# Kernel optimization log

Hardware: AMD Instinct MI355X
Metric: run time of the kernel (lower is better)

The kernel has to match this reference:

```python
import jax, jax.numpy as jnp
import numpy as np

C = 384          # input_channels
DH = 768         # dim_hidden
WS = 7           # window size (kernel_size)
NH = 12          # num_heads
HID = 3072       # mlp hidden = dim_hidden * mlp_ratio
NP = WS * WS     # 49 patch tokens
N = NP + 1       # + 1 cls token
SCALE = (C // NH) ** -0.5
REL_DIM = 2 * WS - 1


def _rel_pos_index():
    r = np.arange(WS)
    qx, qy = np.meshgrid(r, r, indexing='ij')
    q = np.stack([qx.ravel(), qy.ravel()], -1)                 # [NP,2], row-major flatten
    rel = q[:, None, :] - q[None, :, :] + WS - 1               # [NP,NP,2], values in [0,2ws-2]
    return jnp.asarray(rel[..., 0] * REL_DIM + rel[..., 1])    # [NP,NP]

REL_IDX = _rel_pos_index()


def layer_norm(x, g, b, eps=1e-5):
    m = jnp.mean(x, axis=-1, keepdims=True)
    v = jnp.var(x, axis=-1, keepdims=True)
    return (x - m) * jax.lax.rsqrt(v + eps) * g + b


def attention(x, w_qkv, w_proj, b_proj, rel_pos=None, mask=None):
    Bx, Nx, Cx = x.shape
    qkv = (x @ w_qkv.T).reshape(Bx, Nx, 3, NH, Cx // NH).transpose(2, 0, 3, 1, 4)
    q, k, v = qkv[0], qkv[1], qkv[2]                           # [B,H,N,d]
    attn = jnp.einsum('bhqd,bhkd->bhqk', q, k) * SCALE
    if rel_pos is not None:
        bias = rel_pos[REL_IDX].transpose(2, 0, 1)[None]       # [1,NH,NP,NP]
        attn = attn.at[:, :, 1:, 1:].add(bias)                 # skip cls token row/col
    if mask is not None:
        attn = attn + mask[:, None]                            # broadcast over heads
    attn = jax.nn.softmax(attn, axis=-1)
    y = jnp.einsum('bhqk,bhkd->bhqd', attn, v).transpose(0, 2, 1, 3).reshape(Bx, Nx, Cx)
    return y @ w_proj.T + b_proj


def setup_inputs() -> dict:
    key = jax.random.key(0)
    ks = jax.random.split(key, 16)
    s = 0.02
    BNW = 2048  # B * num_windows = 32 * 64
    return {
        'out': jax.random.normal(ks[0], (BNW, N, C), jnp.float32),
        'mask': jnp.zeros((BNW, N, N), jnp.float32),
        'g0': jnp.ones((C,), jnp.float32), 'b0': jnp.zeros((C,), jnp.float32),
        'g1': jnp.ones((C,), jnp.float32), 'b1': jnp.zeros((C,), jnp.float32),
        'g2': jnp.ones((C,), jnp.float32), 'b2': jnp.zeros((C,), jnp.float32),
        'ge': jnp.ones((C,), jnp.float32), 'be': jnp.zeros((C,), jnp.float32),
        'w_qkv': jax.random.normal(ks[1], (3 * C, C), jnp.float32) * s,
        'w_proj': jax.random.normal(ks[2], (C, C), jnp.float32) * s,
        'b_proj': jnp.zeros((C,), jnp.float32),
        'rel_pos': jax.random.normal(ks[3], (REL_DIM * REL_DIM, NH), jnp.float32) * s,
        'w_fc1': jax.random.normal(ks[4], (HID, C), jnp.float32) * s,
        'b_fc1': jnp.zeros((HID,), jnp.float32),
        'w_fc2': jax.random.normal(ks[5], (DH, HID), jnp.float32) * s,
        'b_fc2': jnp.zeros((DH,), jnp.float32),
        'w_exp': jax.random.normal(ks[6], (DH, C), jnp.float32) * s,
        'b_exp': jnp.zeros((DH,), jnp.float32),
        'w_lin': jax.random.normal(ks[7], (C, DH), jnp.float32) * s,
        'b_lin': jnp.zeros((C,), jnp.float32),
        'B': 32, 'H': 56, 'W': 56,
    }


def reference(out, mask, g0, b0, g1, b1, g2, b2, ge, be,
              w_qkv, w_proj, b_proj, rel_pos,
              w_fc1, b_fc1, w_fc2, b_fc2, w_exp, b_exp, w_lin, b_lin,
              B, H, W):
    Cc = out.shape[-1]
    # cls-token attention across windows of each image
    cls = out[:, :1].reshape(B, -1, Cc)                        # [B, nw, C]
    cls = cls + attention(layer_norm(cls, g0, b0), w_qkv, w_proj, b_proj)
    cls = cls.reshape(-1, 1, Cc)
    x = jnp.concatenate([cls, out[:, 1:]], axis=1)             # [B*nw, N, C]
    # windowed patch attention with rel-pos bias + mask
    x = x + attention(layer_norm(x, g1, b1), w_qkv, w_proj, b_proj,
                      rel_pos=rel_pos, mask=mask)
    # expand path: norm -> gelu -> linear (input_channels != dim_hidden)
    identity = jax.nn.gelu(layer_norm(x, ge, be), approximate=False) @ w_exp.T + b_exp
    # mlp path: norm -> fc1 -> gelu -> fc2
    h = layer_norm(x, g2, b2)
    h = jax.nn.gelu(h @ w_fc1.T + b_fc1, approximate=False)
    h = h @ w_fc2.T + b_fc2
    tmp = identity + h                                          # [B*nw, N, DH]
    return tmp @ w_lin.T + b_lin                                # [B*nw, N, C]
```

## Files before the change

### kernel.cpp

```cpp
#include <hip/hip_runtime.h>
#include <hip/hip_bf16.h>
#include <math.h>

#define NHEADS 12
#define NTOK   50
#define NWIN   2048
#define IMGS   32
#define CDIM   384
#define QKVD   1152
#define DHID   768
#define MLPH   3072
#define KTAIL  3456
#define SCALE_F 0.17677669529663687f

typedef short short8 __attribute__((ext_vector_type(8)));
typedef short short4v __attribute__((ext_vector_type(4)));
typedef short short2v __attribute__((ext_vector_type(2)));
typedef float f32x4  __attribute__((ext_vector_type(4)));
typedef __hip_bfloat16 bf16;

__device__ __forceinline__ float gelu_f(float x){
  return 0.5f*x*(1.0f+erff(x*0.7071067811865476f));
}
__device__ __forceinline__ short bfs(float x){
  bf16 h = __float2bfloat16(x); return *(short*)&h;
}

__global__ void cvt4_kernel(const float* s0, bf16* d0, int n0,
                            const float* s1, bf16* d1, int n1,
                            const float* s2, bf16* d2, int n2,
                            const float* s3, bf16* d3, int n3){
  int stride = gridDim.x*blockDim.x, g = blockIdx.x*blockDim.x + threadIdx.x;
  for (int i=g; i<n0; i+=stride) d0[i] = __float2bfloat16(s0[i]);
  for (int i=g; i<n1; i+=stride) d1[i] = __float2bfloat16(s1[i]);
  for (int i=g; i<n2; i+=stride) d2[i] = __float2bfloat16(s2[i]);
  for (int i=g; i<n3; i+=stride) d3[i] = __float2bfloat16(s3[i]);
}

__global__ __launch_bounds__(256) void transpose_cvt_kernel(const float* __restrict__ src,
    bf16* __restrict__ dst, int R, int Cc){
  __shared__ float tile[32][33];
  int bx = blockIdx.x, by = blockIdx.y;
  int c = threadIdx.x & 31, r0 = threadIdx.x >> 5;
  #pragma unroll
  for (int rr = r0; rr < 32; rr += 8)
    tile[rr][c] = src[(size_t)(by*32+rr)*Cc + bx*32 + c];
  __syncthreads();
  #pragma unroll
  for (int rr = r0; rr < 32; rr += 8)
    dst[(size_t)(bx*32+rr)*R + by*32 + c] = __float2bfloat16(tile[c][rr]);
}

__global__ void bias_combine_kernel(const float* __restrict__ wlin,
    const float* __restrict__ b_lin, const float* __restrict__ b_exp,
    const float* __restrict__ b_fc2, float* __restrict__ biasc){
  int i = blockIdx.x*blockDim.x + threadIdx.x;
  if (i >= CDIM) return;
  float s = b_lin[i];
  for (int d=0; d<DHID; d++) s += wlin[(size_t)i*DHID+d]*(b_exp[d]+b_fc2[d]);
  biasc[i] = s;
}

template<bool GELU>
__global__ __launch_bounds__(256) void ln_kernel(const float* __restrict__ x, long ldx,
    const float* __restrict__ g, const float* __restrict__ b,
    bf16* __restrict__ y, int rows)
{
  int row = blockIdx.x*4 + (threadIdx.x>>6);
  if (row >= rows) return;
  int l = threadIdx.x & 63;
  const float2* xr = (const float2*)(x + (size_t)row*ldx);
  float2 v[3]; float s = 0.f;
  #pragma unroll
  for (int j=0;j<3;j++){ v[j] = xr[l + 64*j]; s += v[j].x + v[j].y; }
  #pragma unroll
  for (int off=32; off; off>>=1) s += __shfl_xor(s, off, 64);
  float mean = s * (1.0f/384.0f);
  float vs = 0.f;
  #pragma unroll
  for (int j=0;j<3;j++){ float dx=v[j].x-mean, dy=v[j].y-mean; vs += dx*dx+dy*dy; }
  #pragma unroll
  for (int off=32; off; off>>=1) vs += __shfl_xor(vs, off, 64);
  float rstd = rsqrtf(vs*(1.0f/384.0f) + 1e-5f);
  short2v* yr = (short2v*)(y + (size_t)row*384);
  const float2* gv = (const float2*)g; const float2* bv = (const float2*)b;
  #pragma unroll
  for (int j=0;j<3;j++){
    float2 gg = gv[l+64*j], bb = bv[l+64*j];
    float o0 = (v[j].x-mean)*rstd*gg.x + bb.x;
    float o1 = (v[j].y-mean)*rstd*gg.y + bb.y;
    if (GELU){ o0 = gelu_f(o0); o1 = gelu_f(o1); }
    short2v pk; pk[0]=bfs(o0); pk[1]=bfs(o1);
    yr[l+64*j] = pk;
  }
}

__global__ __launch_bounds__(256) void ln_dual_kernel(const float* __restrict__ x,
    const float* __restrict__ ge, const float* __restrict__ be,
    const float* __restrict__ g2, const float* __restrict__ b2,
    bf16* __restrict__ yeo, long lde, bf16* __restrict__ y2o, int rows)
{
  int row = blockIdx.x*4 + (threadIdx.x>>6);
  if (row >= rows) return;
  int l = threadIdx.x & 63;
  const float2* xr = (const float2*)(x + (size_t)row*384);
  float2 v[3]; float s = 0.f;
  #pragma unroll
  for (int j=0;j<3;j++){ v[j] = xr[l + 64*j]; s += v[j].x + v[j].y; }
  #pragma unroll
  for (int off=32; off; off>>=1) s += __shfl_xor(s, off, 64);
  float mean = s * (1.0f/384.0f);
  float vs = 0.f;
  #pragma unroll
  for (int j=0;j<3;j++){ float dx=v[j].x-mean, dy=v[j].y-mean; vs += dx*dx+dy*dy; }
  #pragma unroll
  for (int off=32; off; off>>=1) vs += __shfl_xor(vs, off, 64);
  float rstd = rsqrtf(vs*(1.0f/384.0f) + 1e-5f);
  short2v* ye = (short2v*)(yeo + (size_t)row*lde);
  short2v* y2 = (short2v*)(y2o + (size_t)row*384);
  const float2* gev = (const float2*)ge; const float2* bev = (const float2*)be;
  const float2* g2v = (const float2*)g2; const float2* b2v = (const float2*)b2;
  #pragma unroll
  for (int j=0;j<3;j++){
    float n0 = (v[j].x-mean)*rstd, n1 = (v[j].y-mean)*rstd;
    float2 gg = gev[l+64*j], bb = bev[l+64*j];
    short2v pe; pe[0]=bfs(gelu_f(n0*gg.x+bb.x)); pe[1]=bfs(gelu_f(n1*gg.y+bb.y));
    ye[l+64*j] = pe;
    gg = g2v[l+64*j]; bb = b2v[l+64*j];
    short2v p2; p2[0]=bfs(n0*gg.x+bb.x); p2[1]=bfs(n1*gg.y+bb.y);
    y2[l+64*j] = p2;
  }
}

template<bool OUT_BF16, bool BIAS, int RES, bool GELU>
__device__ __forceinline__ void gemm_dev(
    const bf16* __restrict__ A, const bf16* __restrict__ B, void* Cv,
    const float* __restrict__ bias, const void* res,
    int M, int N, int K, int ldc, int ldres)
{
  __shared__ short As[3][128*32];
  __shared__ short Bs[3][128*32];
  const int t  = threadIdx.x;
  const int l  = t & 63;
  const int w  = t >> 6;
  const int wr = w >> 1, wc = w & 1;
  const int lr = l & 15, kg = l >> 4;

  const int nwg = gridDim.x * gridDim.y;
  const int lin = blockIdx.y * gridDim.x + blockIdx.x;
  const int q8 = nwg >> 3, r8 = nwg & 7;
  const int xcd = lin & 7, slot = lin >> 3;
  const int swz = (xcd < r8) ? (xcd*(q8+1) + slot) : (r8*(q8+1) + (xcd-r8)*q8 + slot);
  const int by = swz / gridDim.x, bx = swz - by*gridDim.x;

  const int bm = by * 128, bn = bx * 128;
  const short* Ag = (const short*)A;
  const short* Bg = (const short*)B;

  const int eo0 = w*1024 + l*8;
  const int rowS0 = eo0 >> 5, colS0 = eo0 & 31;
  const int eo1 = eo0 + 512;
  const int rowS1 = eo1 >> 5, colS1 = eo1 & 31;

  #define STAGE(k0, b) do { \
    __builtin_amdgcn_global_load_lds( \
      (const __attribute__((address_space(1))) void*)&Ag[(size_t)(bm+rowS0)*K + (k0) + colS0], \
      (__attribute__((address_space(3))) void*)((char*)&As[b][0] + w*2048), 16, 0, 0); \
    __builtin_amdgcn_global_load_lds( \
      (const __attribute__((address_space(1))) void*)&Bg[(size_t)(bn+rowS0)*K + (k0) + colS0], \
      (__attribute__((address_space(3))) void*)((char*)&Bs[b][0] + w*2048), 16, 0, 0); \
    __builtin_amdgcn_global_load_lds( \
      (const __attribute__((address_space(1))) void*)&Ag[(size_t)(bm+rowS1)*K + (k0) + colS1], \
      (__attribute__((address_space(3))) void*)((char*)&As[b][0] + w*2048 + 1024), 16, 0, 0); \
    __builtin_amdgcn_global_load_lds( \
      (const __attribute__((address_space(1))) void*)&Bg[(size_t)(bn+rowS1)*K + (k0) + colS1], \
      (__attribute__((address_space(3))) void*)((char*)&Bs[b][0] + w*2048 + 1024), 16, 0, 0); \
  } while(0)

  f32x4 acc[4][4] = {};

  STAGE(0, 0);
  STAGE(32, 1);
  asm volatile("s_waitcnt vmcnt(4)" ::: "memory");
  __builtin_amdgcn_s_barrier();

  int cur = 0, nb = 2;
  for (int k0 = 0; k0 < K; k0 += 32) {
    const bool more = (k0 + 64 < K);
    if (more) STAGE(k0 + 64, nb);

    short8 af[4], bfm[4];
    #pragma unroll
    for (int m=0;m<4;m++) af[m]  = *(const short8*)(&As[cur][(wr*64 + m*16 + lr)*32 + kg*8]);
    #pragma unroll
    for (int n=0;n<4;n++) bfm[n] = *(const short8*)(&Bs[cur][(wc*64 + n*16 + lr)*32 + kg*8]);
    __builtin_amdgcn_s_setprio(1);
    #pragma unroll
    for (int m=0;m<4;m++)
      #pragma unroll
      for (int n=0;n<4;n++)
        acc[m][n] = __builtin_amdgcn_mfma_f32_16x16x32_bf16(af[m], bfm[n], acc[m][n], 0,0,0);
    __builtin_amdgcn_s_setprio(0);

    if (more) { asm volatile("s_waitcnt vmcnt(4)" ::: "memory"); }
    else      { asm volatile("s_waitcnt vmcnt(0)" ::: "memory"); }
    __builtin_amdgcn_s_barrier();
    cur = (cur==2) ? 0 : cur+1;
    nb  = (nb==2)  ? 0 : nb+1;
  }
  #undef STAGE

  #pragma unroll
  for (int m=0;m<4;m++){
    int row0 = bm + wr*64 + m*16 + kg*4;
    #pragma unroll
    for (int n=0;n<4;n++){
      int col = bn + wc*64 + n*16 + lr;
      float bv = BIAS ? bias[col] : 0.0f;
      #pragma unroll
      for (int r=0;r<4;r++){
        float val = acc[m][n][r] + bv;
        if (RES == 1) val += ((const float*)res)[(size_t)(row0+r)*ldres + col];
        if (GELU) val = gelu_f(val);
        if (OUT_BF16) ((bf16*)Cv)[(size_t)(row0+r)*ldc + col] = __float2bfloat16(val);
        else          ((float*)Cv)[(size_t)(row0+r)*ldc + col] = val;
      }
    }
  }
}

#define GEMM_K(NAME, OB, BI, RE, GE) \
__global__ __launch_bounds__(256) void NAME( \
    const bf16* __restrict__ A, const bf16* __restrict__ B, void* Cv, \
    const float* __restrict__ bias, const void* res, \
    int M, int N, int K, int ldc, int ldres){ \
  gemm_dev<OB,BI,RE,GE>(A,B,Cv,bias,res,M,N,K,ldc,ldres); }

GEMM_K(gemm_qkv_k,  true,  false, 0, false)
GEMM_K(gemm_proj_k, false, true,  1, false)
GEMM_K(gemm_fc1_k,  true,  true,  0, true)
GEMM_K(gemm_tail_k, false, true,  0, false)
GEMM_K(gemm_wcmb_k, true,  false, 0, false)

__global__ __launch_bounds__(256) void attn_cls_kernel(const bf16* __restrict__ qkv,
                                                       bf16* __restrict__ y)
{
  int img = blockIdx.x, h = blockIdx.y;
  __shared__ float q[64][33], k[64][33], v[64][33];
  __shared__ float s[64][65];
  int t = threadIdx.x;
  for (int idx=t; idx<64*32; idx+=256){
    int i = idx>>5, d = idx&31;
    const bf16* base = qkv + ((size_t)(img*64+i))*QKVD + h*32 + d;
    q[i][d] = __bfloat162float(base[0]);
    k[i][d] = __bfloat162float(base[384]);
    v[i][d] = __bfloat162float(base[768]);
  }
  __syncthreads();
  for (int idx=t; idx<64*64; idx+=256){
    int i = idx>>6, j = idx&63;
    float a = 0.f;
    #pragma unroll
    for (int d=0; d<32; d++) a += q[i][d]*k[j][d];
    s[i][j] = a * SCALE_F;
  }
  __syncthreads();
  if (t < 64){
    float m = -1e30f;
    for (int j=0;j<64;j++) m = fmaxf(m, s[t][j]);
    float sum = 0.f;
    for (int j=0;j<64;j++){ float e = __expf(s[t][j]-m); s[t][j]=e; sum+=e; }
    float inv = 1.0f/sum;
    for (int j=0;j<64;j++) s[t][j] *= inv;
  }
  __syncthreads();
  for (int idx=t; idx<64*32; idx+=256){
    int i = idx>>5, d = idx&31;
    float a = 0.f;
    for (int j=0;j<64;j++) a += s[i][j]*v[j][d];
    y[((size_t)(img*64+i))*CDIM + h*32 + d] = __float2bfloat16(a);
  }
}

__global__ __launch_bounds__(64) void attn_win_mfma(const bf16* __restrict__ qkv,
    const float* __restrict__ mask, const float* __restrict__ rel_pos,
    bf16* __restrict__ y)
{
  const int lw = blockIdx.x, h = blockIdx.y;
  const int l = threadIdx.x;
  const int lr = l & 15, kg = l >> 4;
  __shared__ short Plds[64*72];
  __shared__ short VTl[32*72];
  __shared__ float rp[169];

  const size_t tok0 = (size_t)lw * NTOK;
  const short* qbase = (const short*)qkv;

  for (int i=l; i<169; i+=64) rp[i] = rel_pos[i*NHEADS + h];

  short8 qf[4], kf[4];
  #pragma unroll
  for (int n=0;n<4;n++){
    int qt = 16*n + lr;
    if (qt < 50) qf[n] = *(const short8*)&qbase[(tok0+qt)*QKVD + h*32 + kg*8];
    else         qf[n] = short8(0);
  }
  #pragma unroll
  for (int m=0;m<4;m++){
    int kt = 16*m + lr;
    if (kt < 50) kf[m] = *(const short8*)&qbase[(tok0+kt)*QKVD + 384 + h*32 + kg*8];
    else         kf[m] = short8(0);
  }

  {
    short vv[32];
    if (l < 50){
      const short8* vp = (const short8*)&qbase[(tok0+l)*QKVD + 768 + h*32];
      #pragma unroll
      for (int jj=0;jj<4;jj++){ short8 xv = vp[jj];
        #pragma unroll
        for (int e=0;e<8;e++) vv[jj*8+e] = xv[e]; }
    } else {
      #pragma unroll
      for (int d=0; d<32; d++) vv[d]=0;
    }
    #pragma unroll
    for (int d=0; d<32; d++) VTl[d*72 + l] = vv[d];
  }

  f32x4 sacc[4][4] = {};
  #pragma unroll
  for (int m=0;m<4;m++)
    #pragma unroll
    for (int n=0;n<4;n++)
      sacc[m][n] = __builtin_amdgcn_mfma_f32_16x16x32_bf16(kf[m], qf[n], sacc[m][n], 0,0,0);

  const float* mrow = mask + (size_t)lw*2500;
  float sv[4][4][4];
  #pragma unroll
  for (int m=0;m<4;m++){
    #pragma unroll
    for (int r=0;r<4;r++){
      int kt = 16*m + 4*kg + r;
      #pragma unroll
      for (int n=0;n<4;n++){
        int qt = 16*n + lr;
        float a;
        if (kt < 50 && qt < 50){
          a = sacc[m][n][r] * SCALE_F;
          if (kt>=1 && qt>=1){
            int qi=qt-1, kj=kt-1;
            int ridx = ((qi/7)-(kj/7)+6)*13 + (qi%7)-(kj%7)+6;
            a += rp[ridx];
          }
          a += mrow[qt*50+kt];
        } else a = -1e30f;
        sv[m][r][n] = a;
      }
    }
  }

  #pragma unroll
  for (int n=0;n<4;n++){
    float mx = -1e30f;
    #pragma unroll
    for (int m=0;m<4;m++)
      #pragma unroll
      for (int r=0;r<4;r++) mx = fmaxf(mx, sv[m][r][n]);
    mx = fmaxf(mx, __shfl_xor(mx, 16));
    mx = fmaxf(mx, __shfl_xor(mx, 32));
    float sum = 0.f;
    float pv[4][4];
    #pragma unroll
    for (int m=0;m<4;m++)
      #pragma unroll
      for (int r=0;r<4;r++){ float p = __expf(sv[m][r][n]-mx); pv[m][r]=p; sum+=p; }
    sum += __shfl_xor(sum, 16);
    sum += __shfl_xor(sum, 32);
    float inv = 1.0f/sum;
    int qrow = (16*n + lr)*72;
    #pragma unroll
    for (int m=0;m<4;m++){
      short4v pk;
      #pragma unroll
      for (int r=0;r<4;r++) pk[r] = bfs(pv[m][r]*inv);
      *(short4v*)&Plds[qrow + 16*m + 4*kg] = pk;
    }
  }
  __syncthreads();

  f32x4 oacc[2][4] = {};
  #pragma unroll
  for (int ks=0; ks<2; ks++){
    short8 pf[4];
    #pragma unroll
    for (int n=0;n<4;n++)
      pf[n] = *(const short8*)&Plds[(16*n+lr)*72 + 32*ks + kg*8];
    #pragma unroll
    for (int md=0; md<2; md++){
      short8 vf = *(const short8*)&VTl[(16*md+lr)*72 + 32*ks + kg*8];
      #pragma unroll
      for (int n=0;n<4;n++)
        oacc[md][n] = __builtin_amdgcn_mfma_f32_16x16x32_bf16(vf, pf[n], oacc[md][n], 0,0,0);
    }
  }

  short* yb = (short*)y;
  #pragma unroll
  for (int n=0;n<4;n++){
    int qt = 16*n + lr;
    if (qt >= 50) continue;
    #pragma unroll
    for (int md=0; md<2; md++){
      short4v pk;
      #pragma unroll
      for (int r=0;r<4;r++) pk[r] = bfs(oacc[md][n][r]);
      *(short4v*)&yb[(tok0+qt)*CDIM + h*32 + 16*md + 4*kg] = pk;
    }
  }
}

extern "C" void kernel_launch(void* const* d_in, const int* in_sizes, int n_in,
                              void* d_out, int out_size, void* d_ws, size_t ws_size,
                              hipStream_t stream)
{
  const float* x_in   = (const float*)d_in[0];
  const float* maskp  = (const float*)d_in[1];
  const float* g0 = (const float*)d_in[2];  const float* b0 = (const float*)d_in[3];
  const float* g1 = (const float*)d_in[4];  const float* b1 = (const float*)d_in[5];
  const float* g2 = (const float*)d_in[6];  const float* b2 = (const float*)d_in[7];
  const float* ge = (const float*)d_in[8];  const float* be = (const float*)d_in[9];
  const float* w_qkv = (const float*)d_in[10];
  const float* w_proj= (const float*)d_in[11];
  const float* b_proj= (const float*)d_in[12];
  const float* rel_pos=(const float*)d_in[13];
  const float* w_fc1 = (const float*)d_in[14];
  const float* b_fc1 = (const float*)d_in[15];
  const float* w_fc2 = (const float*)d_in[16];
  const float* b_fc2 = (const float*)d_in[17];
  const float* w_exp = (const float*)d_in[18];
  const float* b_exp = (const float*)d_in[19];
  const float* w_lin = (const float*)d_in[20];
  const float* b_lin = (const float*)d_in[21];
  float* dout = (float*)d_out;

  const size_t NT = (size_t)NWIN * NTOK;

  size_t off = 0;
  auto alloc = [&](size_t bytes)->void* {
    void* p = (char*)d_ws + off;
    off += (bytes + 255) & ~(size_t)255;
    return p;
  };

  bf16* wqkv_b = (bf16*)alloc((size_t)QKVD*CDIM*2);
  bf16* wproj_b= (bf16*)alloc((size_t)CDIM*CDIM*2);
  bf16* wfc1_b = (bf16*)alloc((size_t)MLPH*CDIM*2);
  bf16* wlin_b = (bf16*)alloc((size_t)CDIM*DHID*2);
  bf16* wexpT_b= (bf16*)alloc((size_t)CDIM*DHID*2);
  bf16* wfc2T_b= (bf16*)alloc((size_t)MLPH*DHID*2);
  bf16* W_comb = (bf16*)alloc((size_t)CDIM*KTAIL*2);
  float* biasc = (float*)alloc((size_t)CDIM*4);
  float* xb    = (float*)alloc(NT*CDIM*4);
  bf16* clsln  = (bf16*)alloc((size_t)NWIN*CDIM*2);
  bf16* qkvcls = (bf16*)alloc((size_t)NWIN*QKVD*2);
  bf16* ycls   = (bf16*)alloc((size_t)NWIN*CDIM*2);

  int CH_W = 2048;
  const size_t per_window = 537600ull;
  while (CH_W > 128 && off + (size_t)CH_W*per_window + 16384 > ws_size) CH_W >>= 1;
  const int CH_T = CH_W * NTOK;

  bf16*  xln   = (bf16*) alloc((size_t)CH_T*CDIM*2);
  bf16*  qkvc  = (bf16*) alloc((size_t)CH_T*QKVD*2);
  bf16*  ybfc  = (bf16*) alloc((size_t)CH_T*CDIM*2);
  bf16*  h1ext = (bf16*) alloc((size_t)CH_T*KTAIL*2);

  cvt4_kernel<<<512, 256, 0, stream>>>(
      w_qkv, wqkv_b, QKVD*CDIM,  w_proj, wproj_b, CDIM*CDIM,
      w_fc1, wfc1_b, MLPH*CDIM,  w_lin,  wlin_b,  CDIM*DHID);
  transpose_cvt_kernel<<<dim3(CDIM/32, DHID/32), 256, 0, stream>>>(w_exp, wexpT_b, DHID, CDIM);
  transpose_cvt_kernel<<<dim3(MLPH/32, DHID/32), 256, 0, stream>>>(w_fc2, wfc2T_b, DHID, MLPH);
  bias_combine_kernel<<<6, 64, 0, stream>>>(w_lin, b_lin, b_exp, b_fc2, biasc);
  gemm_wcmb_k<<<dim3(CDIM/128, CDIM/128), 256, 0, stream>>>(
      wlin_b, wexpT_b, W_comb, nullptr, nullptr, CDIM, CDIM, DHID, KTAIL, 0);
  gemm_wcmb_k<<<dim3(MLPH/128, CDIM/128), 256, 0, stream>>>(
      wlin_b, wfc2T_b, W_comb + 384, nullptr, nullptr, CDIM, MLPH, DHID, KTAIL, 0);

  hipMemcpyAsync(xb, x_in, NT*CDIM*4, hipMemcpyDeviceToDevice, stream);

  ln_kernel<false><<<NWIN/4, 256, 0, stream>>>(x_in, (long)NTOK*CDIM, g0, b0, clsln, NWIN);
  gemm_qkv_k<<<dim3(QKVD/128, NWIN/128), 256, 0, stream>>>(
      clsln, wqkv_b, qkvcls, nullptr, nullptr, NWIN, QKVD, CDIM, QKVD, 0);
  attn_cls_kernel<<<dim3(IMGS, NHEADS), 256, 0, stream>>>(qkvcls, ycls);
  gemm_proj_k<<<dim3(CDIM/128, NWIN/128), 256, 0, stream>>>(
      ycls, wproj_b, xb, b_proj, x_in, NWIN, CDIM, CDIM, NTOK*CDIM, NTOK*CDIM);

  const int nch = NWIN / CH_W;
  for (int c = 0; c < nch; c++){
    int w0 = c * CH_W;
    size_t t0 = (size_t)w0 * NTOK;
    float* xbc = xb + t0*CDIM;
    float* doutc = dout + t0*CDIM;
    int MT = CH_T, MB = CH_T/128;

    ln_kernel<false><<<MT/4, 256, 0, stream>>>(xbc, CDIM, g1, b1, xln, MT);
    gemm_qkv_k<<<dim3(QKVD/128, MB), 256, 0, stream>>>(
        xln, wqkv_b, qkvc, nullptr, nullptr, MT, QKVD, CDIM, QKVD, 0);
    attn_win_mfma<<<dim3(CH_W, NHEADS), 64, 0, stream>>>(
        qkvc, maskp + (size_t)w0*2500, rel_pos, ybfc);
    gemm_proj_k<<<dim3(CDIM/128, MB), 256, 0, stream>>>(
        ybfc, wproj_b, xbc, b_proj, xbc, MT, CDIM, CDIM, CDIM, CDIM);

    ln_dual_kernel<<<MT/4, 256, 0, stream>>>(xbc, ge, be, g2, b2, h1ext, KTAIL, ybfc, MT);

    gemm_fc1_k<<<dim3(MLPH/128, MB), 256, 0, stream>>>(
        ybfc, wfc1_b, h1ext + 384, b_fc1, nullptr, MT, MLPH, CDIM, KTAIL, 0);

    gemm_tail_k<<<dim3(CDIM/128, MB), 256, 0, stream>>>(
        h1ext, W_comb, doutc, biasc, nullptr, MT, CDIM, KTAIL, CDIM, 0);
  }
}
```

Measured before the change: 1.826 ms.

## Deepen GEMM LDS pipeline to five stages and use tanh-approximated GELU

Makes the bf16 MFMA GEMM prefetch four K-tiles ahead through a five-buffer LDS ring instead of two ahead in three buffers, with an explicit drain at the end. The aim is to hide more global-load latency. It also raises LDS use to 80 KB per block, which can cut occupancy. Separately, the exact erf GELU is replaced by the tanh approximation computed with __expf, which is cheaper but numerically differs from the reference's exact GELU.

```diff
diff --git a/kernel.cpp b/kernel.cpp
--- a/kernel.cpp
+++ b/kernel.cpp
@@ -20,7 +20,9 @@
 typedef __hip_bfloat16 bf16;
 
 __device__ __forceinline__ float gelu_f(float x){
-  return 0.5f*x*(1.0f+erff(x*0.7071067811865476f));
+  float z = 0.7978845608028654f*(x + 0.044715f*x*x*x);
+  float e = __expf(2.0f*z);
+  return 0.5f*x*(1.0f + (1.0f - 2.0f/(e+1.0f)));
 }
 __device__ __forceinline__ short bfs(float x){
   bf16 h = __float2bfloat16(x); return *(short*)&h;
@@ -138,8 +140,8 @@
     const float* __restrict__ bias, const void* res,
     int M, int N, int K, int ldc, int ldres)
 {
-  __shared__ short As[3][128*32];
-  __shared__ short Bs[3][128*32];
+  __shared__ short As[5][128*32];
+  __shared__ short Bs[5][128*32];
   const int t  = threadIdx.x;
   const int l  = t & 63;
   const int w  = t >> 6;
@@ -177,38 +179,52 @@
       (__attribute__((address_space(3))) void*)((char*)&Bs[b][0] + w*2048 + 1024), 16, 0, 0); \
   } while(0)
 
+  #define COMPUTE(buf) do { \
+    short8 af[4], bfm[4]; \
+    _Pragma("unroll") \
+    for (int m=0;m<4;m++) af[m]  = *(const short8*)(&As[buf][(wr*64 + m*16 + lr)*32 + kg*8]); \
+    _Pragma("unroll") \
+    for (int n=0;n<4;n++) bfm[n] = *(const short8*)(&Bs[buf][(wc*64 + n*16 + lr)*32 + kg*8]); \
+    __builtin_amdgcn_s_setprio(1); \
+    _Pragma("unroll") \
+    for (int m=0;m<4;m++) \
+      _Pragma("unroll") \
+      for (int n=0;n<4;n++) \
+        acc[m][n] = __builtin_amdgcn_mfma_f32_16x16x32_bf16(af[m], bfm[n], acc[m][n], 0,0,0); \
+    __builtin_amdgcn_s_setprio(0); \
+  } while(0)
+
   f32x4 acc[4][4] = {};
-
-  STAGE(0, 0);
-  STAGE(32, 1);
+  const int nt = K >> 5;
+
+  STAGE(0, 0); STAGE(32, 1); STAGE(64, 2); STAGE(96, 3);
+  asm volatile("s_waitcnt vmcnt(12)" ::: "memory");
+  __builtin_amdgcn_s_barrier();
+
+  int cur = 0;
+  for (int tt = 0; tt < nt-4; ++tt){
+    int nb = cur+4; if (nb >= 5) nb -= 5;
+    STAGE((tt+4)*32, nb);
+    COMPUTE(cur);
+    asm volatile("s_waitcnt vmcnt(12)" ::: "memory");
+    __builtin_amdgcn_s_barrier();
+    cur = (cur==4) ? 0 : cur+1;
+  }
+  COMPUTE(cur);
+  asm volatile("s_waitcnt vmcnt(8)" ::: "memory");
+  __builtin_amdgcn_s_barrier();
+  cur = (cur==4) ? 0 : cur+1;
+  COMPUTE(cur);
   asm volatile("s_waitcnt vmcnt(4)" ::: "memory");
   __builtin_amdgcn_s_barrier();
-
-  int cur = 0, nb = 2;
-  for (int k0 = 0; k0 < K; k0 += 32) {
-    const bool more = (k0 + 64 < K);
-    if (more) STAGE(k0 + 64, nb);
-
-    short8 af[4], bfm[4];
-    #pragma unroll
-    for (int m=0;m<4;m++) af[m]  = *(const short8*)(&As[cur][(wr*64 + m*16 + lr)*32 + kg*8]);
-    #pragma unroll
-    for (int n=0;n<4;n++) bfm[n] = *(const short8*)(&Bs[cur][(wc*64 + n*16 + lr)*32 + kg*8]);
-    __builtin_amdgcn_s_setprio(1);
-    #pragma unroll
-    for (int m=0;m<4;m++)
-      #pragma unroll
-      for (int n=0;n<4;n++)
-        acc[m][n] = __builtin_amdgcn_mfma_f32_16x16x32_bf16(af[m], bfm[n], acc[m][n], 0,0,0);
-    __builtin_amdgcn_s_setprio(0);
-
-    if (more) { asm volatile("s_waitcnt vmcnt(4)" ::: "memory"); }
-    else      { asm volatile("s_waitcnt vmcnt(0)" ::: "memory"); }
-    __builtin_amdgcn_s_barrier();
-    cur = (cur==2) ? 0 : cur+1;
-    nb  = (nb==2)  ? 0 : nb+1;
-  }
+  cur = (cur==4) ? 0 : cur+1;
+  COMPUTE(cur);
+  asm volatile("s_waitcnt vmcnt(0)" ::: "memory");
+  __builtin_amdgcn_s_barrier();
+  cur = (cur==4) ? 0 : cur+1;
+  COMPUTE(cur);
   #undef STAGE
+  #undef COMPUTE
 
   #pragma unroll
   for (int m=0;m<4;m++){
```

After: 2.140 ms. 1.17x slower.

## Add 256-row 512-thread GEMM kernels and switch GELU to tanh approximation

Applied to the files above, without the earlier changes.

Adds a new GEMM template with 256-row tiles, 8 waves, triple-buffered direct global-to-LDS loads, and a 256-wide N tile for fc1. It replaces the 128x128 GEMMs in the per-chunk loop (qkv, proj, fc1, tail) to raise data reuse per block and reduce block count. Separately, GELU is changed from exact erf to the tanh approximation via exp, which cuts epilogue cost but departs from the reference's approximate=False semantics. Larger tiles halve the number of M blocks, which may hurt occupancy or tail balance if chunk sizes are small.

```diff
diff --git a/kernel.cpp b/kernel.cpp
--- a/kernel.cpp
+++ b/kernel.cpp
@@ -20,7 +20,9 @@
 typedef __hip_bfloat16 bf16;
 
 __device__ __forceinline__ float gelu_f(float x){
-  return 0.5f*x*(1.0f+erff(x*0.7071067811865476f));
+  float z = 0.7978845608028654f*(x + 0.044715f*x*x*x);
+  float e = __expf(2.0f*z);
+  return 0.5f*x*(1.0f + (1.0f - 2.0f/(e+1.0f)));
 }
 __device__ __forceinline__ short bfs(float x){
   bf16 h = __float2bfloat16(x); return *(short*)&h;
@@ -131,6 +133,135 @@
     y2[l+64*j] = p2;
   }
 }
+
+template<int BN, bool OUT_BF16, bool BIAS, int RES, bool GELU>
+__device__ __forceinline__ void g256_dev(
+    const bf16* __restrict__ A, const bf16* __restrict__ B, void* Cv,
+    const float* __restrict__ bias, const void* res,
+    int M, int N, int K, int ldc, int ldres)
+{
+  constexpr int WN    = BN/64;
+  constexpr int WM    = 8/WN;
+  constexpr int MREP  = 256/(16*WM);
+  constexpr int BINST = BN/128;
+  constexpr int V     = 2 + BINST;
+
+  __shared__ short As[3][256*32];
+  __shared__ short Bs[3][BN*32];
+
+  const int t  = threadIdx.x;
+  const int l  = t & 63;
+  const int w  = t >> 6;
+  const int wr = w / WN, wc = w % WN;
+  const int lr = l & 15, kg = l >> 4;
+  const int wrow = wr * (MREP*16);
+
+  const int nwg = gridDim.x * gridDim.y;
+  const int lin = blockIdx.y * gridDim.x + blockIdx.x;
+  const int q8 = nwg >> 3, r8 = nwg & 7;
+  const int xcd = lin & 7, slot = lin >> 3;
+  const int swz = (xcd < r8) ? (xcd*(q8+1) + slot) : (r8*(q8+1) + (xcd-r8)*q8 + slot);
+  const int by = swz / gridDim.x, bx = swz - by*gridDim.x;
+  const int bm = by * 256, bn = bx * BN;
+
+  const short* Ag = (const short*)A;
+  const short* Bg = (const short*)B;
+
+  const int srow = l >> 2;
+  const int scol = ((l&3) ^ ((l>>3)&3)) * 8;
+
+  #define STAGE(k0, b) do { \
+    _Pragma("unroll") \
+    for (int p=0;p<2;p++){ \
+      int j = w*2+p; \
+      __builtin_amdgcn_global_load_lds( \
+        (const __attribute__((address_space(1))) void*)&Ag[(size_t)(bm + j*16 + srow)*K + (k0) + scol], \
+        (__attribute__((address_space(3))) void*)((char*)&As[b][0] + j*1024), 16, 0, 0); \
+    } \
+    _Pragma("unroll") \
+    for (int p=0;p<BINST;p++){ \
+      int j = w*BINST+p; \
+      __builtin_amdgcn_global_load_lds( \
+        (const __attribute__((address_space(1))) void*)&Bg[(size_t)(bn + j*16 + srow)*K + (k0) + scol], \
+        (__attribute__((address_space(3))) void*)((char*)&Bs[b][0] + j*1024), 16, 0, 0); \
+    } \
+  } while(0)
+
+  #define SWZ(row) ((row)*64 + (((kg ^ (((row)>>1)&3)))<<4))
+
+  #define COMPUTE(buf) do { \
+    short8 af[MREP], bfm[4]; \
+    _Pragma("unroll") \
+    for (int mf=0; mf<MREP; mf++){ \
+      int rrow = wrow + mf*16 + lr; \
+      af[mf] = *(const short8*)((const char*)&As[buf][0] + SWZ(rrow)); \
+    } \
+    _Pragma("unroll") \
+    for (int nf=0; nf<4; nf++){ \
+      int rrow = wc*64 + nf*16 + lr; \
+      bfm[nf] = *(const short8*)((const char*)&Bs[buf][0] + SWZ(rrow)); \
+    } \
+    __builtin_amdgcn_s_setprio(1); \
+    _Pragma("unroll") \
+    for (int mf=0; mf<MREP; mf++) \
+      _Pragma("unroll") \
+      for (int nf=0; nf<4; nf++) \
+        acc[mf][nf] = __builtin_amdgcn_mfma_f32_16x16x32_bf16(af[mf], bfm[nf], acc[mf][nf], 0,0,0); \
+    __builtin_amdgcn_s_setprio(0); \
+  } while(0)
+
+  f32x4 acc[MREP][4] = {};
+
+  STAGE(0, 0);
+  STAGE(32, 1);
+  asm volatile("s_waitcnt vmcnt(%0)" :: "i"(V) : "memory");
+  __builtin_amdgcn_s_barrier();
+
+  int cur = 0, nb = 2;
+  for (int k0 = 0; k0 < K; k0 += 32) {
+    const bool more = (k0 + 64 < K);
+    if (more) STAGE(k0 + 64, nb);
+    COMPUTE(cur);
+    if (more) { asm volatile("s_waitcnt vmcnt(%0)" :: "i"(V) : "memory"); }
+    else      { asm volatile("s_waitcnt vmcnt(0)" ::: "memory"); }
+    __builtin_amdgcn_s_barrier();
+    cur = (cur==2) ? 0 : cur+1;
+    nb  = (nb==2)  ? 0 : nb+1;
+  }
+  #undef STAGE
+  #undef COMPUTE
+  #undef SWZ
+
+  #pragma unroll
+  for (int mf=0; mf<MREP; mf++){
+    int row0 = bm + wrow + mf*16 + kg*4;
+    #pragma unroll
+    for (int nf=0; nf<4; nf++){
+      int col = bn + wc*64 + nf*16 + lr;
+      float bv = BIAS ? bias[col] : 0.0f;
+      #pragma unroll
+      for (int r=0;r<4;r++){
+        float val = acc[mf][nf][r] + bv;
+        if (RES == 1) val += ((const float*)res)[(size_t)(row0+r)*ldres + col];
+        if (GELU) val = gelu_f(val);
+        if (OUT_BF16) ((bf16*)Cv)[(size_t)(row0+r)*ldc + col] = __float2bfloat16(val);
+        else          ((float*)Cv)[(size_t)(row0+r)*ldc + col] = val;
+      }
+    }
+  }
+}
+
+#define G256_K(NAME, BN, OB, BI, RE, GE) \
+__global__ __launch_bounds__(512, 2) void NAME( \
+    const bf16* __restrict__ A, const bf16* __restrict__ B, void* Cv, \
+    const float* __restrict__ bias, const void* res, \
+    int M, int N, int K, int ldc, int ldres){ \
+  g256_dev<BN,OB,BI,RE,GE>(A,B,Cv,bias,res,M,N,K,ldc,ldres); }
+
+G256_K(g256_qkv,  128, true,  false, 0, false)
+G256_K(g256_proj, 128, false, true,  1, false)
+G256_K(g256_fc1,  256, true,  true,  0, true)
+G256_K(g256_tail, 128, false, true,  0, false)
 
 template<bool OUT_BF16, bool BIAS, int RES, bool GELU>
 __device__ __forceinline__ void gemm_dev(
@@ -238,8 +369,6 @@
 
 GEMM_K(gemm_qkv_k,  true,  false, 0, false)
 GEMM_K(gemm_proj_k, false, true,  1, false)
-GEMM_K(gemm_fc1_k,  true,  true,  0, true)
-GEMM_K(gemm_tail_k, false, true,  0, false)
 GEMM_K(gemm_wcmb_k, true,  false, 0, false)
 
 __global__ __launch_bounds__(256) void attn_cls_kernel(const bf16* __restrict__ qkv,
@@ -502,22 +631,22 @@
     size_t t0 = (size_t)w0 * NTOK;
     float* xbc = xb + t0*CDIM;
     float* doutc = dout + t0*CDIM;
-    int MT = CH_T, MB = CH_T/128;
+    int MT = CH_T, MB = CH_T/256;
 
     ln_kernel<false><<<MT/4, 256, 0, stream>>>(xbc, CDIM, g1, b1, xln, MT);
-    gemm_qkv_k<<<dim3(QKVD/128, MB), 256, 0, stream>>>(
+    g256_qkv<<<dim3(QKVD/128, MB), 512, 0, stream>>>(
         xln, wqkv_b, qkvc, nullptr, nullptr, MT, QKVD, CDIM, QKVD, 0);
     attn_win_mfma<<<dim3(CH_W, NHEADS), 64, 0, stream>>>(
         qkvc, maskp + (size_t)w0*2500, rel_pos, ybfc);
-    gemm_proj_k<<<dim3(CDIM/128, MB), 256, 0, stream>>>(
+    g256_proj<<<dim3(CDIM/128, MB), 512, 0, stream>>>(
         ybfc, wproj_b, xbc, b_proj, xbc, MT, CDIM, CDIM, CDIM, CDIM);
 
     ln_dual_kernel<<<MT/4, 256, 0, stream>>>(xbc, ge, be, g2, b2, h1ext, KTAIL, ybfc, MT);
 
-    gemm_fc1_k<<<dim3(MLPH/128, MB), 256, 0, stream>>>(
+    g256_fc1<<<dim3(MLPH/256, MB), 512, 0, stream>>>(
         ybfc, wfc1_b, h1ext + 384, b_fc1, nullptr, MT, MLPH, CDIM, KTAIL, 0);
 
-    gemm_tail_k<<<dim3(CDIM/128, MB), 256, 0, stream>>>(
+    g256_tail<<<dim3(CDIM/128, MB), 512, 0, stream>>>(
         h1ext, W_comb, doutc, biasc, nullptr, MT, CDIM, KTAIL, CDIM, 0);
   }
 }
```

Measured after the change: 1.947 ms. 6.7% more time.
